# Kernel tuning notes

Hardware: AMD Instinct MI355X
Metric: run time of the kernel (lower is better)

The kernel has to match this reference:

```python
import jax, jax.numpy as jnp
import numpy as np

HID = 64  # hidden_channels


def _conv1x1(x, w, b):
    # x: [B,C,H,W], w: [O,C], b: [O] -> [B,O,H,W] (1x1 conv = per-pixel linear)
    return jnp.einsum('bchw,oc->bohw', x, w) + b[None, :, None, None]


def setup_inputs() -> dict:
    key = jax.random.key(0)
    ks = jax.random.split(key, 9)
    B, C, H, W = 64, 1, 86, 86
    return {
        'x': jax.random.normal(ks[0], (B, C, H, W), dtype=jnp.float32),
        'Wq': jax.random.normal(ks[1], (HID, C), dtype=jnp.float32) * 0.1,
        'bq': jax.random.normal(ks[2], (HID,), dtype=jnp.float32) * 0.1,
        'Wk': jax.random.normal(ks[3], (HID, C), dtype=jnp.float32) * 0.1,
        'bk': jax.random.normal(ks[4], (HID,), dtype=jnp.float32) * 0.1,
        'Wv': jax.random.normal(ks[5], (HID, C), dtype=jnp.float32) * 0.1,
        'bv': jax.random.normal(ks[6], (HID,), dtype=jnp.float32) * 0.1,
        'Wo': jax.random.normal(ks[7], (C, HID), dtype=jnp.float32) * 0.1,
        'bo': jax.random.normal(ks[8], (C,), dtype=jnp.float32) * 0.1,
    }


def reference(x, Wq, bq, Wk, bk, Wv, bv, Wo, bo):
    B, C, H, W = x.shape
    N = H * W  # 7396 spatial tokens
    Q = _conv1x1(x, Wq, bq).reshape(B, HID, N)  # [B,hid,N]
    K = _conv1x1(x, Wk, bk).reshape(B, HID, N)
    V = _conv1x1(x, Wv, bv).reshape(B, HID, N)
    # scores: Q @ K^T over spatial dim -> [B,hid,hid] (channel attention)
    scores = jnp.einsum('bhn,bgn->bhg', Q, K) / jnp.sqrt(jnp.float32(HID))
    attn = jax.nn.softmax(scores, axis=-1)  # [B,hid,hid]
    out = jnp.einsum('bhg,bgn->bhn', attn, V).reshape(B, HID, H, W)
    return _conv1x1(out, Wo, bo)  # [B,C,H,W]
```

## Files before the change

kernel.cpp:

```cpp
#include <hip/hip_runtime.h>
#include <math.h>

#define HID 64

__global__ __launch_bounds__(1024) void spatial_attn_fused(
    const float* __restrict__ x,
    const float* __restrict__ Wq, const float* __restrict__ bq,
    const float* __restrict__ Wk, const float* __restrict__ bk,
    const float* __restrict__ Wv, const float* __restrict__ bv,
    const float* __restrict__ Wo, const float* __restrict__ bo,
    float* __restrict__ out,
    int N)
{
    const int b = blockIdx.x;
    const int tid = threadIdx.x;
    const int nthreads = blockDim.x;
    const float* xb = x + (size_t)b * N;
    float* yb = out + (size_t)b * N;

    float s1 = 0.f, s2 = 0.f;
    const int nvec = N >> 2;
    const float4* xv = reinterpret_cast<const float4*>(xb);
    for (int i = tid; i < nvec; i += nthreads) {
        float4 v = xv[i];
        s1 += v.x + v.y + v.z + v.w;
        s2 += v.x * v.x + v.y * v.y + v.z * v.z + v.w * v.w;
    }
    for (int i = (nvec << 2) + tid; i < N; i += nthreads) {
        float v = xb[i];
        s1 += v; s2 += v * v;
    }
    for (int off = 32; off > 0; off >>= 1) {
        s1 += __shfl_down(s1, off);
        s2 += __shfl_down(s2, off);
    }
    __shared__ float lds1[16], lds2[16];
    __shared__ float sS1, sS2, sAlpha, sBeta;
    const int wave = tid >> 6, lane = tid & 63;
    const int nwaves = nthreads >> 6;
    if (lane == 0) { lds1[wave] = s1; lds2[wave] = s2; }
    __syncthreads();
    if (tid == 0) {
        float a = 0.f, c = 0.f;
        for (int w = 0; w < nwaves; ++w) { a += lds1[w]; c += lds2[w]; }
        sS1 = a; sS2 = c;
    }
    __syncthreads();
    const float S1 = sS1, S2 = sS2;

    if (tid < HID) {
        const int h = tid;
        const float wqh = Wq[h], bqh = bq[h];
        const float scale = 0.125f;
        const float fN = (float)N;

        float m = -INFINITY;
        for (int g = 0; g < HID; ++g) {
            float wkg = Wk[g], bkg = bk[g];
            float sc = (wqh * wkg * S2 + (wqh * bkg + bqh * wkg) * S1 + bqh * bkg * fN) * scale;
            m = fmaxf(m, sc);
        }
        float sum = 0.f, sumA = 0.f, sumB = 0.f;
        for (int g = 0; g < HID; ++g) {
            float wkg = Wk[g], bkg = bk[g];
            float sc = (wqh * wkg * S2 + (wqh * bkg + bqh * wkg) * S1 + bqh * bkg * fN) * scale;
            float e = __expf(sc - m);
            sum += e;
            sumA += e * Wv[g];
            sumB += e * bv[g];
        }
        const float inv = 1.f / sum;
        const float woh = Wo[h];
        float ca = woh * (sumA * inv);
        float cb = woh * (sumB * inv);
        for (int off = 32; off > 0; off >>= 1) {
            ca += __shfl_down(ca, off);
            cb += __shfl_down(cb, off);
        }
        if (h == 0) { sAlpha = ca; sBeta = cb + bo[0]; }
    }
    __syncthreads();
    const float alpha = sAlpha, beta = sBeta;

    float4* yv = reinterpret_cast<float4*>(yb);
    for (int i = tid; i < nvec; i += nthreads) {
        float4 v = xv[i];
        float4 r;
        r.x = fmaf(alpha, v.x, beta);
        r.y = fmaf(alpha, v.y, beta);
        r.z = fmaf(alpha, v.z, beta);
        r.w = fmaf(alpha, v.w, beta);
        yv[i] = r;
    }
    for (int i = (nvec << 2) + tid; i < N; i += nthreads) {
        yb[i] = fmaf(alpha, xb[i], beta);
    }
}

extern "C" void kernel_launch(void* const* d_in, const int* in_sizes, int n_in,
                              void* d_out, int out_size, void* d_ws, size_t ws_size,
                              hipStream_t stream) {
    const float* x  = (const float*)d_in[0];
    const float* Wq = (const float*)d_in[1];
    const float* bq = (const float*)d_in[2];
    const float* Wk = (const float*)d_in[3];
    const float* bk = (const float*)d_in[4];
    const float* Wv = (const float*)d_in[5];
    const float* bv = (const float*)d_in[6];
    const float* Wo = (const float*)d_in[7];
    const float* bo = (const float*)d_in[8];
    float* out = (float*)d_out;

    const int B = 64;
    const int N = in_sizes[0] / B;

    spatial_attn_fused<<<B, 1024, 0, stream>>>(x, Wq, bq, Wk, bk, Wv, bv, Wo, bo, out, N);
}
```

Before: 15.25 us.

## Split output pass across chunked blocks and parallelize softmax over all waves

Launches four blocks per batch, each redundantly computing the batch statistics and softmax coefficients, then writing only its quarter of the output. The per-row softmax is spread across all 16 waves, using wave shuffles over the 64 keys instead of a serial loop in one wave. This aims to use more CUs and shorten the serial softmax section. The cost is reading x four times for the reductions and an extra LDS reduction barrier.

```diff
diff --git a/kernel.cpp b/kernel.cpp
--- a/kernel.cpp
+++ b/kernel.cpp
@@ -2,8 +2,10 @@
 #include <math.h>
 
 #define HID 64
+#define CHUNKS 4
+#define NTHREADS 1024
 
-__global__ __launch_bounds__(1024) void spatial_attn_fused(
+__global__ __launch_bounds__(NTHREADS) void spatial_attn_fused(
     const float* __restrict__ x,
     const float* __restrict__ Wq, const float* __restrict__ bq,
     const float* __restrict__ Wk, const float* __restrict__ bk,
@@ -12,78 +14,87 @@
     float* __restrict__ out,
     int N)
 {
-    const int b = blockIdx.x;
-    const int tid = threadIdx.x;
-    const int nthreads = blockDim.x;
-    const float* xb = x + (size_t)b * N;
-    float* yb = out + (size_t)b * N;
+    const int bid   = blockIdx.x;
+    const int b     = bid & 63;
+    const int chunk = bid >> 6;
+    const int tid   = threadIdx.x;
+    const float* xb = x   + (size_t)b * N;
+    float*       yb = out + (size_t)b * N;
 
     float s1 = 0.f, s2 = 0.f;
     const int nvec = N >> 2;
     const float4* xv = reinterpret_cast<const float4*>(xb);
-    for (int i = tid; i < nvec; i += nthreads) {
+    for (int i = tid; i < nvec; i += NTHREADS) {
         float4 v = xv[i];
-        s1 += v.x + v.y + v.z + v.w;
+        s1 += (v.x + v.y) + (v.z + v.w);
         s2 += v.x * v.x + v.y * v.y + v.z * v.z + v.w * v.w;
     }
-    for (int i = (nvec << 2) + tid; i < N; i += nthreads) {
+    for (int i = (nvec << 2) + tid; i < N; i += NTHREADS) {
         float v = xb[i];
         s1 += v; s2 += v * v;
     }
+    #pragma unroll
     for (int off = 32; off > 0; off >>= 1) {
         s1 += __shfl_down(s1, off);
         s2 += __shfl_down(s2, off);
     }
-    __shared__ float lds1[16], lds2[16];
+    __shared__ float lds1[16], lds2[16], ldsA[16], ldsB[16];
     __shared__ float sS1, sS2, sAlpha, sBeta;
     const int wave = tid >> 6, lane = tid & 63;
-    const int nwaves = nthreads >> 6;
     if (lane == 0) { lds1[wave] = s1; lds2[wave] = s2; }
     __syncthreads();
     if (tid == 0) {
         float a = 0.f, c = 0.f;
-        for (int w = 0; w < nwaves; ++w) { a += lds1[w]; c += lds2[w]; }
+        #pragma unroll
+        for (int w = 0; w < NTHREADS / 64; ++w) { a += lds1[w]; c += lds2[w]; }
         sS1 = a; sS2 = c;
     }
     __syncthreads();
     const float S1 = sS1, S2 = sS2;
 
-    if (tid < HID) {
-        const int h = tid;
+    const float scale = 0.125f;
+    const float fN = (float)N;
+    const float wk_g = Wk[lane], bk_g = bk[lane];
+    const float wv_g = Wv[lane], bv_g = bv[lane];
+    float cA = 0.f, cB = 0.f;
+    #pragma unroll
+    for (int j = 0; j < HID / (NTHREADS / 64); ++j) {
+        const int h = wave * (HID / (NTHREADS / 64)) + j;
         const float wqh = Wq[h], bqh = bq[h];
-        const float scale = 0.125f;
-        const float fN = (float)N;
-
-        float m = -INFINITY;
-        for (int g = 0; g < HID; ++g) {
-            float wkg = Wk[g], bkg = bk[g];
-            float sc = (wqh * wkg * S2 + (wqh * bkg + bqh * wkg) * S1 + bqh * bkg * fN) * scale;
-            m = fmaxf(m, sc);
+        const float P = (wqh * S2 + bqh * S1) * scale;
+        const float Q = (wqh * S1 + bqh * fN) * scale;
+        const float sc = P * wk_g + Q * bk_g;
+        float m = sc;
+        #pragma unroll
+        for (int off = 32; off > 0; off >>= 1) m = fmaxf(m, __shfl_xor(m, off));
+        const float e = __expf(sc - m);
+        float s = e, sA = e * wv_g, sB = e * bv_g;
+        #pragma unroll
+        for (int off = 32; off > 0; off >>= 1) {
+            s  += __shfl_xor(s,  off);
+            sA += __shfl_xor(sA, off);
+            sB += __shfl_xor(sB, off);
         }
-        float sum = 0.f, sumA = 0.f, sumB = 0.f;
-        for (int g = 0; g < HID; ++g) {
-            float wkg = Wk[g], bkg = bk[g];
-            float sc = (wqh * wkg * S2 + (wqh * bkg + bqh * wkg) * S1 + bqh * bkg * fN) * scale;
-            float e = __expf(sc - m);
-            sum += e;
-            sumA += e * Wv[g];
-            sumB += e * bv[g];
-        }
-        const float inv = 1.f / sum;
+        const float inv = 1.f / s;
         const float woh = Wo[h];
-        float ca = woh * (sumA * inv);
-        float cb = woh * (sumB * inv);
-        for (int off = 32; off > 0; off >>= 1) {
-            ca += __shfl_down(ca, off);
-            cb += __shfl_down(cb, off);
-        }
-        if (h == 0) { sAlpha = ca; sBeta = cb + bo[0]; }
+        cA += woh * (sA * inv);
+        cB += woh * (sB * inv);
+    }
+    if (lane == 0) { ldsA[wave] = cA; ldsB[wave] = cB; }
+    __syncthreads();
+    if (tid == 0) {
+        float a = 0.f, c = 0.f;
+        #pragma unroll
+        for (int w = 0; w < NTHREADS / 64; ++w) { a += ldsA[w]; c += ldsB[w]; }
+        sAlpha = a; sBeta = c + bo[0];
     }
     __syncthreads();
     const float alpha = sAlpha, beta = sBeta;
 
+    const int i0 = (chunk * nvec) / CHUNKS;
+    const int i1 = ((chunk + 1) * nvec) / CHUNKS;
     float4* yv = reinterpret_cast<float4*>(yb);
-    for (int i = tid; i < nvec; i += nthreads) {
+    for (int i = i0 + tid; i < i1; i += NTHREADS) {
         float4 v = xv[i];
         float4 r;
         r.x = fmaf(alpha, v.x, beta);
@@ -92,8 +103,9 @@
         r.w = fmaf(alpha, v.w, beta);
         yv[i] = r;
     }
-    for (int i = (nvec << 2) + tid; i < N; i += nthreads) {
-        yb[i] = fmaf(alpha, xb[i], beta);
+    if (chunk == CHUNKS - 1) {
+        for (int i = (nvec << 2) + tid; i < N; i += NTHREADS)
+            yb[i] = fmaf(alpha, xb[i], beta);
     }
 }
 
@@ -114,5 +126,6 @@
     const int B = 64;
     const int N = in_sizes[0] / B;
 
-    spatial_attn_fused<<<B, 1024, 0, stream>>>(x, Wq, bq, Wk, bk, Wv, bv, Wo, bo, out, N);
+    spatial_attn_fused<<<B * CHUNKS, NTHREADS, 0, stream>>>(
+        x, Wq, bq, Wk, bk, Wv, bv, Wo, bo, out, N);
 }
```

Result: faster. 12.47 us (-18.2%).
